# Kernel tuning notes

Hardware: AMD Instinct MI355X
Metric: run time of the kernel (lower is better)

The kernel has to match this reference:

```python
import jax, jax.numpy as jnp
import numpy as np

N_STATE = 1024
N_HEAD = 16
HEAD_DIM = N_STATE // N_HEAD
SEQLENS = [1024, 896, 768, 640, 512, 384, 896, 1024]  # sum = 6144
TOTAL = sum(SEQLENS)


def setup_inputs() -> dict:
    key = jax.random.key(0)
    ks = jax.random.split(key, 8)
    s = 0.02
    cu = jnp.asarray(np.concatenate([[0], np.cumsum(SEQLENS)]), dtype=jnp.int32)
    return {
        "x": jax.random.normal(ks[0], (TOTAL, N_STATE), jnp.float32),
        "cu_seqlens": cu,
        "Wq": jax.random.normal(ks[1], (N_STATE, N_STATE), jnp.float32) * s,
        "bq": jax.random.normal(ks[2], (N_STATE,), jnp.float32) * s,
        "Wk": jax.random.normal(ks[3], (N_STATE, N_STATE), jnp.float32) * s,
        "Wv": jax.random.normal(ks[4], (N_STATE, N_STATE), jnp.float32) * s,
        "bv": jax.random.normal(ks[5], (N_STATE,), jnp.float32) * s,
        "Wo": jax.random.normal(ks[6], (N_STATE, N_STATE), jnp.float32) * s,
        "bo": jax.random.normal(ks[7], (N_STATE,), jnp.float32) * s,
    }


def reference(x, cu_seqlens, Wq, bq, Wk, Wv, bv, Wo, bo):
    # cu_seqlens is a static (host) quantity in the original (used via .tolist())
    cu = np.asarray(jax.device_get(cu_seqlens))
    seqlens = cu[1:] - cu[:-1]
    B = len(seqlens)
    Lmax = int(seqlens.max())

    q = x @ Wq.T + bq              # [T, n_state]
    k = x @ Wk.T                   # key has no bias
    v = x @ Wv.T + bv

    # static pad/unpad index maps (honoring the ragged structure)
    ar = np.arange(Lmax)
    valid = ar[None, :] < seqlens[:, None]             # [B, Lmax]
    idx = np.where(valid, cu[:-1, None] + ar[None, :], 0)
    unpad_idx = np.nonzero(valid.reshape(-1))[0]       # flat positions of real tokens
    valid_j = jnp.asarray(valid)

    def pad(t):  # [T, n_state] -> [B, Lmax, H, D], zeros in padding
        p = jnp.where(valid_j[:, :, None], t[idx], 0.0)
        return p.reshape(B, Lmax, N_HEAD, HEAD_DIM)

    qp, kp, vp = pad(q), pad(k), pad(v)
    scale = HEAD_DIM ** -0.5
    # torch adds the bool mask (True->1.0) after masked_fill(mask==0, -max):
    # valid keys get +1.0 (softmax-invariant shift), invalid keys get -finfo.max
    big_neg = jnp.finfo(x.dtype).max
    add_mask = jnp.where(valid_j, 1.0, -big_neg)[:, None, None, :]  # [B,1,1,Lmax]

    scores = jnp.einsum("bqhd,bkhd->bhqk", qp, kp) * scale + add_mask
    weights = jax.nn.softmax(scores, axis=-1)
    ctx = jnp.einsum("bhqk,bkhd->bqhd", weights, vp)   # [B, Lmax, H, D]
    ctx_flat = ctx.reshape(B * Lmax, N_STATE)[unpad_idx]  # [T, n_state]
    return ctx_flat @ Wo.T + bo
```

## Files before the change

kernel.cpp:

```cpp
#include <hip/hip_runtime.h>

typedef unsigned short u16;
typedef unsigned int u32;
typedef __attribute__((ext_vector_type(8))) short bf16x8;
typedef __attribute__((ext_vector_type(4))) float f32x4;

#define MFMA_BF16(a, b, c) __builtin_amdgcn_mfma_f32_16x16x32_bf16((a), (b), (c), 0, 0, 0)

#define QSCALE 0.18033688011112042f

__device__ __forceinline__ u16 f2bf(float f) {
    union { float f; unsigned u; } v; v.f = f;
    return (u16)((v.u + 0x7FFFu + ((v.u >> 16) & 1u)) >> 16);
}

__device__ __forceinline__ u32 pkbf(float a, float b) {
    union { float f; unsigned u; } x, y; x.f = a; y.f = b;
    return ((x.u + 0x8000u) >> 16) | ((y.u + 0x8000u) & 0xFFFF0000u);
}

__device__ __forceinline__ void async16(const void* g, void* l) {
    __builtin_amdgcn_global_load_lds(
        (const __attribute__((address_space(1))) void*)g,
        (__attribute__((address_space(3))) void*)l, 16, 0, 0);
}

__global__ __launch_bounds__(256) void cvt_all(
    const float* __restrict__ x, const float* __restrict__ Wq, const float* __restrict__ Wk,
    const float* __restrict__ Wv, const float* __restrict__ Wo,
    u16* __restrict__ xb, u16* __restrict__ Wqb, u16* __restrict__ Wkb,
    u16* __restrict__ Wvb, u16* __restrict__ Wob) {
    int b = blockIdx.x;
    const float* src; u16* dst; int base;
    if (b < 6144)      { src = x;  dst = xb;  base = b; }
    else if (b < 7168) { src = Wq; dst = Wqb; base = b - 6144; }
    else if (b < 8192) { src = Wk; dst = Wkb; base = b - 7168; }
    else if (b < 9216) { src = Wv; dst = Wvb; base = b - 8192; }
    else               { src = Wo; dst = Wob; base = b - 9216; }
    int i = base * 256 + threadIdx.x;
    float4 v = ((const float4*)src)[i];
    unsigned long long pk = (unsigned long long)f2bf(v.x)
                          | ((unsigned long long)f2bf(v.y) << 16)
                          | ((unsigned long long)f2bf(v.z) << 32)
                          | ((unsigned long long)f2bf(v.w) << 48);
    *(unsigned long long*)(dst + (size_t)i * 4) = pk;
}

__global__ __launch_bounds__(256) void gemm_qkv(
    const u16* __restrict__ xb,
    const u16* __restrict__ Wqb, const u16* __restrict__ Wkb, const u16* __restrict__ Wvb,
    const float* __restrict__ bq, const float* __restrict__ bv,
    u16* __restrict__ qb, u16* __restrict__ kb, u16* __restrict__ vbT) {
    __shared__ __align__(16) u16 As[128 * 64];
    __shared__ __align__(16) u16 Bs[128 * 64];
    const int tid = threadIdx.x;

    const int fid = blockIdx.x;
    const int xcd = fid & 7;
    const int slot = fid >> 3;
    const int mloc = slot % 6;
    const int nidx = slot / 6;
    const int m0 = (xcd * 6 + mloc) << 7;
    const int buf = nidx >> 3;
    const int n0 = (nidx & 7) << 7;
    const u16* __restrict__ W = (buf == 0) ? Wqb : (buf == 1) ? Wkb : Wvb;

    const int rr = tid >> 3;
    const int cg = tid & 7;
    const int wv = tid >> 6, lane = tid & 63, g = lane >> 4, c = lane & 15;
    const int wm = (wv & 1) << 6, wn = (wv >> 1) << 6;

    const int sw = (cg ^ (rr & 7)) << 3;
    const u16* gA[4]; const u16* gB[4];
#pragma unroll
    for (int r = 0; r < 4; ++r) {
        gA[r] = xb + (size_t)(m0 + (r << 5) + rr) * 1024 + sw;
        gB[r] = W + (size_t)(n0 + (r << 5) + rr) * 1024 + sw;
    }

    f32x4 zero = {0.f, 0.f, 0.f, 0.f};
    f32x4 acc[4][4];
#pragma unroll
    for (int i = 0; i < 4; ++i)
#pragma unroll
        for (int j = 0; j < 4; ++j) acc[i][j] = zero;

    for (int kt = 0; kt < 16; ++kt) {
        const int k0 = kt << 6;
        __syncthreads();
#pragma unroll
        for (int r = 0; r < 4; ++r) {
            async16(gA[r] + k0, &As[(r << 11) + tid * 8]);
            async16(gB[r] + k0, &Bs[(r << 11) + tid * 8]);
        }
        __syncthreads();
#pragma unroll
        for (int ks = 0; ks < 2; ++ks) {
            bf16x8 af[4], bb[4];
#pragma unroll
            for (int i = 0; i < 4; ++i) {
                int ra = wm + (i << 4) + c;
                af[i] = *(const bf16x8*)(&As[ra * 64 + ((((ks << 2) + g) ^ (ra & 7)) << 3)]);
                int rb = wn + (i << 4) + c;
                bb[i] = *(const bf16x8*)(&Bs[rb * 64 + ((((ks << 2) + g) ^ (rb & 7)) << 3)]);
            }
#pragma unroll
            for (int i = 0; i < 4; ++i)
#pragma unroll
                for (int j = 0; j < 4; ++j) acc[i][j] = MFMA_BF16(af[i], bb[j], acc[i][j]);
        }
    }

    if (buf == 0) {
#pragma unroll
        for (int j = 0; j < 4; ++j) {
            int col = n0 + wn + (j << 4) + c;
            float bias = bq[col];
#pragma unroll
            for (int i = 0; i < 4; ++i) {
                int rowb = m0 + wm + (i << 4) + (g << 2);
#pragma unroll
                for (int r = 0; r < 4; ++r)
                    qb[(size_t)(rowb + r) * 1024 + col] = f2bf((acc[i][j][r] + bias) * QSCALE);
            }
        }
    } else if (buf == 1) {
#pragma unroll
        for (int j = 0; j < 4; ++j) {
            int col = n0 + wn + (j << 4) + c;
#pragma unroll
            for (int i = 0; i < 4; ++i) {
                int rowb = m0 + wm + (i << 4) + (g << 2);
#pragma unroll
                for (int r = 0; r < 4; ++r)
                    kb[(size_t)(rowb + r) * 1024 + col] = f2bf(acc[i][j][r]);
            }
        }
    } else {
#pragma unroll
        for (int j = 0; j < 4; ++j) {
            int col = n0 + wn + (j << 4) + c;
            float bias = bv[col];
#pragma unroll
            for (int i = 0; i < 4; ++i) {
                int trow = m0 + wm + (i << 4) + (g << 2);
                unsigned long long pk =
                      (unsigned long long)f2bf(acc[i][j][0] + bias)
                    | ((unsigned long long)f2bf(acc[i][j][1] + bias) << 16)
                    | ((unsigned long long)f2bf(acc[i][j][2] + bias) << 32)
                    | ((unsigned long long)f2bf(acc[i][j][3] + bias) << 48);
                *(unsigned long long*)(vbT + (size_t)col * 6144 + trow) = pk;
            }
        }
    }
}

__global__ __launch_bounds__(256) void gemm_out(
    const u16* __restrict__ ctxb, const u16* __restrict__ Wob,
    const float* __restrict__ bo, float* __restrict__ out) {
    __shared__ __align__(16) u16 As[64 * 64];
    __shared__ __align__(16) u16 Bs[64 * 64];
    const int tid = threadIdx.x;

    const int fid = blockIdx.x;
    const int xcd = fid & 7;
    const int slot = fid >> 3;
    const int mloc = slot % 12;
    const int nidx = slot / 12;
    const int m0 = (xcd * 12 + mloc) << 6;
    const int n0 = nidx << 6;

    const int rr = tid >> 3, cg = tid & 7;
    const int wv = tid >> 6, lane = tid & 63, g = lane >> 4, c = lane & 15;
    const int wm = (wv & 1) << 5, wn = (wv >> 1) << 5;

    const int sw = (cg ^ (rr & 7)) << 3;
    const u16* gA[2]; const u16* gB[2];
#pragma unroll
    for (int r = 0; r < 2; ++r) {
        gA[r] = ctxb + (size_t)(m0 + (r << 5) + rr) * 1024 + sw;
        gB[r] = Wob + (size_t)(n0 + (r << 5) + rr) * 1024 + sw;
    }

    f32x4 zero = {0.f, 0.f, 0.f, 0.f};
    f32x4 acc[2][2];
#pragma unroll
    for (int i = 0; i < 2; ++i)
#pragma unroll
        for (int j = 0; j < 2; ++j) acc[i][j] = zero;

    for (int kt = 0; kt < 16; ++kt) {
        const int k0 = kt << 6;
        __syncthreads();
#pragma unroll
        for (int r = 0; r < 2; ++r) {
            async16(gA[r] + k0, &As[(r << 11) + tid * 8]);
            async16(gB[r] + k0, &Bs[(r << 11) + tid * 8]);
        }
        __syncthreads();
#pragma unroll
        for (int ks = 0; ks < 2; ++ks) {
            bf16x8 af[2], bb[2];
#pragma unroll
            for (int i = 0; i < 2; ++i) {
                int ra = wm + (i << 4) + c;
                af[i] = *(const bf16x8*)(&As[ra * 64 + ((((ks << 2) + g) ^ (ra & 7)) << 3)]);
                int rb = wn + (i << 4) + c;
                bb[i] = *(const bf16x8*)(&Bs[rb * 64 + ((((ks << 2) + g) ^ (rb & 7)) << 3)]);
            }
#pragma unroll
            for (int i = 0; i < 2; ++i)
#pragma unroll
                for (int j = 0; j < 2; ++j) acc[i][j] = MFMA_BF16(af[i], bb[j], acc[i][j]);
        }
    }

#pragma unroll
    for (int j = 0; j < 2; ++j) {
        int col = n0 + wn + (j << 4) + c;
        float bias = bo[col];
#pragma unroll
        for (int i = 0; i < 2; ++i) {
            int rowb = m0 + wm + (i << 4) + (g << 2);
#pragma unroll
            for (int r = 0; r < 4; ++r)
                out[(size_t)(rowb + r) * 1024 + col] = acc[i][j][r] + bias;
        }
    }
}

__global__ __launch_bounds__(256) void attn_kernel(const u16* __restrict__ qb,
                                                   const u16* __restrict__ kb,
                                                   const u16* __restrict__ vbT,
                                                   u16* __restrict__ ctxb) {
    __shared__ __align__(16) u16 Ks[128 * 64];
    __shared__ __align__(16) u16 Vs[64 * 128];
    __shared__ __align__(16) u16 Ps[4 * 2048];

    const int tid = threadIdx.x;
    const int fid = blockIdx.x;
    const int xcd = fid & 7;
    const int slot = fid >> 3;
    const int h = (xcd << 1) + (slot >= 96 ? 1 : 0);
    const int q0 = (slot % 96) << 6;

    const int cuv[9] = {0, 1024, 1920, 2688, 3328, 3840, 4224, 5120, 6144};
    int s0 = 0, e0 = 6144;
#pragma unroll
    for (int i = 1; i < 8; ++i) {
        if (q0 >= cuv[i]) s0 = cuv[i];
        if (q0 < cuv[i] && cuv[i] < e0) e0 = cuv[i];
    }
    const int ntiles = (e0 - s0) >> 7;

    const int wv = tid >> 6, lane = tid & 63, g = lane >> 4, c = lane & 15;
    const int wrow = wv << 4;

    {
        const int rr = tid >> 3, cg = tid & 7;
#pragma unroll
        for (int r = 0; r < 2; ++r) {
            int row = (r << 5) + rr;
            async16(qb + (size_t)(q0 + row) * 1024 + (h << 6) + ((cg ^ (row & 7)) << 3),
                    Ps + (r << 11) + tid * 8);
        }
    }
    __syncthreads();

    bf16x8 qf[2];
#pragma unroll
    for (int ks = 0; ks < 2; ++ks) {
        int row = wrow + c;
        qf[ks] = *(const bf16x8*)(Ps + row * 64 + ((((ks << 2) + g) ^ (row & 7)) << 3));
    }

    float m_run = -1e30f, l_run = 0.f;
    f32x4 zero = {0.f, 0.f, 0.f, 0.f};
    f32x4 oacc[4];
#pragma unroll
    for (int nt = 0; nt < 4; ++nt) oacc[nt] = zero;

    const int pbase = (wv << 11) + c * 128;
    const int c7 = c & 7;

    for (int kt = 0; kt < ntiles; ++kt) {
        const int kv0 = s0 + (kt << 7);
        __syncthreads();
        {
            const int rr = tid >> 3, cg = tid & 7;
#pragma unroll
            for (int r = 0; r < 4; ++r) {
                int row = (r << 5) + rr;
                async16(kb + (size_t)(kv0 + row) * 1024 + (h << 6) + ((cg ^ (row & 7)) << 3),
                        Ks + (r << 11) + tid * 8);
            }
            const int rr2 = tid >> 4, cg2 = tid & 15;
#pragma unroll
            for (int r = 0; r < 4; ++r) {
                int row = (r << 4) + rr2;
                async16(vbT + (size_t)((h << 6) + row) * 6144 + kv0 + ((cg2 ^ (row & 15)) << 3),
                        Vs + (r << 11) + tid * 8);
            }
        }
        __syncthreads();

        f32x4 st[8];
#pragma unroll
        for (int mt = 0; mt < 8; ++mt) st[mt] = zero;
#pragma unroll
        for (int mt = 0; mt < 8; ++mt) {
            int row = (mt << 4) + c;
            int sw = row & 7;
#pragma unroll
            for (int ks = 0; ks < 2; ++ks) {
                bf16x8 kf = *(const bf16x8*)(&Ks[row * 64 + ((((ks << 2) + g) ^ sw) << 3)]);
                st[mt] = MFMA_BF16(kf, qf[ks], st[mt]);
            }
        }

        float mx = st[0][0];
#pragma unroll
        for (int mt = 0; mt < 8; ++mt)
#pragma unroll
            for (int r = 0; r < 4; ++r) mx = fmaxf(mx, st[mt][r]);
        mx = fmaxf(mx, __shfl_xor(mx, 16, 64));
        mx = fmaxf(mx, __shfl_xor(mx, 32, 64));
        float mnew = fmaxf(m_run, mx);
        float alpha = exp2f(m_run - mnew);
        m_run = mnew;

        float rsum = 0.f;
#pragma unroll
        for (int mt = 0; mt < 8; ++mt) {
            float p0 = exp2f(st[mt][0] - mnew);
            float p1 = exp2f(st[mt][1] - mnew);
            float p2 = exp2f(st[mt][2] - mnew);
            float p3 = exp2f(st[mt][3] - mnew);
            rsum += (p0 + p1) + (p2 + p3);
            int ph = ((mt << 2) + g) ^ (c7 << 1);
            *(uint2*)(Ps + pbase + (ph << 2)) = make_uint2(pkbf(p0, p1), pkbf(p2, p3));
        }
        rsum += __shfl_xor(rsum, 16, 64);
        rsum += __shfl_xor(rsum, 32, 64);
        l_run = l_run * alpha + rsum;

        float al[4];
#pragma unroll
        for (int r = 0; r < 4; ++r) al[r] = __shfl(alpha, (g << 2) + r, 16);
#pragma unroll
        for (int nt = 0; nt < 4; ++nt)
#pragma unroll
            for (int r = 0; r < 4; ++r) oacc[nt][r] *= al[r];

#pragma unroll
        for (int ks = 0; ks < 4; ++ks) {
            int pg = ((ks << 2) + g) ^ c7;
            bf16x8 pf = *(const bf16x8*)(Ps + pbase + (pg << 3));
#pragma unroll
            for (int nt = 0; nt < 4; ++nt) {
                int vrow = (nt << 4) + c;
                bf16x8 vf = *(const bf16x8*)(&Vs[vrow * 128 + ((((ks << 2) + g) ^ (vrow & 15)) << 3)]);
                oacc[nt] = MFMA_BF16(pf, vf, oacc[nt]);
            }
        }
    }

    float inv = 1.0f / l_run;
    float invr[4];
#pragma unroll
    for (int r = 0; r < 4; ++r) invr[r] = __shfl(inv, (g << 2) + r, 16);
#pragma unroll
    for (int r = 0; r < 4; ++r) {
        size_t rowoff = (size_t)(q0 + wrow + (g << 2) + r) * 1024 + (h << 6);
#pragma unroll
        for (int nt = 0; nt < 4; ++nt)
            ctxb[rowoff + (nt << 4) + c] = f2bf(oacc[nt][r] * invr[r]);
    }
}

extern "C" void kernel_launch(void* const* d_in, const int* in_sizes, int n_in,
                              void* d_out, int out_size, void* d_ws, size_t ws_size,
                              hipStream_t stream) {
    const float* x  = (const float*)d_in[0];
    const float* Wq = (const float*)d_in[2];
    const float* bq = (const float*)d_in[3];
    const float* Wk = (const float*)d_in[4];
    const float* Wv = (const float*)d_in[5];
    const float* bv = (const float*)d_in[6];
    const float* Wo = (const float*)d_in[7];
    const float* bo = (const float*)d_in[8];
    float* out = (float*)d_out;

    u16* ws = (u16*)d_ws;
    u16* xb   = ws;
    u16* Wqb  = xb + 6291456;
    u16* Wkb  = Wqb + 1048576;
    u16* Wvb  = Wkb + 1048576;
    u16* Wob  = Wvb + 1048576;
    u16* qb   = Wob + 1048576;
    u16* kb   = qb + 6291456;
    u16* vbT  = kb + 6291456;
    u16* ctxb = xb;

    cvt_all<<<10240, 256, 0, stream>>>(x, Wq, Wk, Wv, Wo, xb, Wqb, Wkb, Wvb, Wob);
    gemm_qkv<<<1152, 256, 0, stream>>>(xb, Wqb, Wkb, Wvb, bq, bv, qb, kb, vbT);
    attn_kernel<<<1536, 256, 0, stream>>>(qb, kb, vbT, ctxb);
    gemm_out<<<1536, 256, 0, stream>>>(ctxb, Wob, bo, out);
}
```

Measured before the change: 233.5 us.

## Double-buffer LDS tiles in QKV, output GEMM and attention kernels

Each of the three main-loop kernels now holds two LDS buffers. The loads for the next K (or KV) tile are issued before the MFMA work on the current tile, and a single barrier sits at the end of each iteration. The aim is to hide global-to-LDS load latency behind compute and to drop one barrier per iteration. In exchange, LDS use per block doubles for the staged tiles (up to about 80KB in attention), which can reduce how many blocks fit on a CU.

```diff
diff --git a/kernel.cpp b/kernel.cpp
--- a/kernel.cpp
+++ b/kernel.cpp
@@ -51,8 +51,8 @@
     const u16* __restrict__ Wqb, const u16* __restrict__ Wkb, const u16* __restrict__ Wvb,
     const float* __restrict__ bq, const float* __restrict__ bv,
     u16* __restrict__ qb, u16* __restrict__ kb, u16* __restrict__ vbT) {
-    __shared__ __align__(16) u16 As[128 * 64];
-    __shared__ __align__(16) u16 Bs[128 * 64];
+    __shared__ __align__(16) u16 As[2][128 * 64];
+    __shared__ __align__(16) u16 Bs[2][128 * 64];
     const int tid = threadIdx.x;
 
     const int fid = blockIdx.x;
@@ -85,30 +85,39 @@
 #pragma unroll
         for (int j = 0; j < 4; ++j) acc[i][j] = zero;
 
+#pragma unroll
+    for (int r = 0; r < 4; ++r) {
+        async16(gA[r], &As[0][(r << 11) + tid * 8]);
+        async16(gB[r], &Bs[0][(r << 11) + tid * 8]);
+    }
+    __syncthreads();
+
     for (int kt = 0; kt < 16; ++kt) {
-        const int k0 = kt << 6;
-        __syncthreads();
-#pragma unroll
-        for (int r = 0; r < 4; ++r) {
-            async16(gA[r] + k0, &As[(r << 11) + tid * 8]);
-            async16(gB[r] + k0, &Bs[(r << 11) + tid * 8]);
-        }
-        __syncthreads();
+        const int cur = kt & 1;
+        if (kt < 15) {
+            const int k0 = (kt + 1) << 6;
+#pragma unroll
+            for (int r = 0; r < 4; ++r) {
+                async16(gA[r] + k0, &As[cur ^ 1][(r << 11) + tid * 8]);
+                async16(gB[r] + k0, &Bs[cur ^ 1][(r << 11) + tid * 8]);
+            }
+        }
 #pragma unroll
         for (int ks = 0; ks < 2; ++ks) {
             bf16x8 af[4], bb[4];
 #pragma unroll
             for (int i = 0; i < 4; ++i) {
                 int ra = wm + (i << 4) + c;
-                af[i] = *(const bf16x8*)(&As[ra * 64 + ((((ks << 2) + g) ^ (ra & 7)) << 3)]);
+                af[i] = *(const bf16x8*)(&As[cur][ra * 64 + ((((ks << 2) + g) ^ (ra & 7)) << 3)]);
                 int rb = wn + (i << 4) + c;
-                bb[i] = *(const bf16x8*)(&Bs[rb * 64 + ((((ks << 2) + g) ^ (rb & 7)) << 3)]);
+                bb[i] = *(const bf16x8*)(&Bs[cur][rb * 64 + ((((ks << 2) + g) ^ (rb & 7)) << 3)]);
             }
 #pragma unroll
             for (int i = 0; i < 4; ++i)
 #pragma unroll
                 for (int j = 0; j < 4; ++j) acc[i][j] = MFMA_BF16(af[i], bb[j], acc[i][j]);
         }
+        __syncthreads();
     }
 
     if (buf == 0) {
@@ -158,8 +167,8 @@
 __global__ __launch_bounds__(256) void gemm_out(
     const u16* __restrict__ ctxb, const u16* __restrict__ Wob,
     const float* __restrict__ bo, float* __restrict__ out) {
-    __shared__ __align__(16) u16 As[64 * 64];
-    __shared__ __align__(16) u16 Bs[64 * 64];
+    __shared__ __align__(16) u16 As[2][64 * 64];
+    __shared__ __align__(16) u16 Bs[2][64 * 64];
     const int tid = threadIdx.x;
 
     const int fid = blockIdx.x;
@@ -189,30 +198,39 @@
 #pragma unroll
         for (int j = 0; j < 2; ++j) acc[i][j] = zero;
 
+#pragma unroll
+    for (int r = 0; r < 2; ++r) {
+        async16(gA[r], &As[0][(r << 11) + tid * 8]);
+        async16(gB[r], &Bs[0][(r << 11) + tid * 8]);
+    }
+    __syncthreads();
+
     for (int kt = 0; kt < 16; ++kt) {
-        const int k0 = kt << 6;
-        __syncthreads();
-#pragma unroll
-        for (int r = 0; r < 2; ++r) {
-            async16(gA[r] + k0, &As[(r << 11) + tid * 8]);
-            async16(gB[r] + k0, &Bs[(r << 11) + tid * 8]);
-        }
-        __syncthreads();
+        const int cur = kt & 1;
+        if (kt < 15) {
+            const int k0 = (kt + 1) << 6;
+#pragma unroll
+            for (int r = 0; r < 2; ++r) {
+                async16(gA[r] + k0, &As[cur ^ 1][(r << 11) + tid * 8]);
+                async16(gB[r] + k0, &Bs[cur ^ 1][(r << 11) + tid * 8]);
+            }
+        }
 #pragma unroll
         for (int ks = 0; ks < 2; ++ks) {
             bf16x8 af[2], bb[2];
 #pragma unroll
             for (int i = 0; i < 2; ++i) {
                 int ra = wm + (i << 4) + c;
-                af[i] = *(const bf16x8*)(&As[ra * 64 + ((((ks << 2) + g) ^ (ra & 7)) << 3)]);
+                af[i] = *(const bf16x8*)(&As[cur][ra * 64 + ((((ks << 2) + g) ^ (ra & 7)) << 3)]);
                 int rb = wn + (i << 4) + c;
-                bb[i] = *(const bf16x8*)(&Bs[rb * 64 + ((((ks << 2) + g) ^ (rb & 7)) << 3)]);
+                bb[i] = *(const bf16x8*)(&Bs[cur][rb * 64 + ((((ks << 2) + g) ^ (rb & 7)) << 3)]);
             }
 #pragma unroll
             for (int i = 0; i < 2; ++i)
 #pragma unroll
                 for (int j = 0; j < 2; ++j) acc[i][j] = MFMA_BF16(af[i], bb[j], acc[i][j]);
         }
+        __syncthreads();
     }
 
 #pragma unroll
@@ -233,8 +251,8 @@
                                                    const u16* __restrict__ kb,
                                                    const u16* __restrict__ vbT,
                                                    u16* __restrict__ ctxb) {
-    __shared__ __align__(16) u16 Ks[128 * 64];
-    __shared__ __align__(16) u16 Vs[64 * 128];
+    __shared__ __align__(16) u16 Ks[2][128 * 64];
+    __shared__ __align__(16) u16 Vs[2][64 * 128];
     __shared__ __align__(16) u16 Ps[4 * 2048];
 
     const int tid = threadIdx.x;
@@ -256,6 +274,23 @@
     const int wv = tid >> 6, lane = tid & 63, g = lane >> 4, c = lane & 15;
     const int wrow = wv << 4;
 
+    auto stageKV = [&](int kv0, int b) {
+        const int rr = tid >> 3, cg = tid & 7;
+#pragma unroll
+        for (int r = 0; r < 4; ++r) {
+            int row = (r << 5) + rr;
+            async16(kb + (size_t)(kv0 + row) * 1024 + (h << 6) + ((cg ^ (row & 7)) << 3),
+                    &Ks[b][(r << 11) + tid * 8]);
+        }
+        const int rr2 = tid >> 4, cg2 = tid & 15;
+#pragma unroll
+        for (int r = 0; r < 4; ++r) {
+            int row = (r << 4) + rr2;
+            async16(vbT + (size_t)((h << 6) + row) * 6144 + kv0 + ((cg2 ^ (row & 15)) << 3),
+                    &Vs[b][(r << 11) + tid * 8]);
+        }
+    };
+
     {
         const int rr = tid >> 3, cg = tid & 7;
 #pragma unroll
@@ -264,6 +299,7 @@
             async16(qb + (size_t)(q0 + row) * 1024 + (h << 6) + ((cg ^ (row & 7)) << 3),
                     Ps + (r << 11) + tid * 8);
         }
+        stageKV(s0, 0);
     }
     __syncthreads();
 
@@ -273,6 +309,7 @@
         int row = wrow + c;
         qf[ks] = *(const bf16x8*)(Ps + row * 64 + ((((ks << 2) + g) ^ (row & 7)) << 3));
     }
+    __syncthreads();
 
     float m_run = -1e30f, l_run = 0.f;
     f32x4 zero = {0.f, 0.f, 0.f, 0.f};
@@ -284,25 +321,8 @@
     const int c7 = c & 7;
 
     for (int kt = 0; kt < ntiles; ++kt) {
-        const int kv0 = s0 + (kt << 7);
-        __syncthreads();
-        {
-            const int rr = tid >> 3, cg = tid & 7;
-#pragma unroll
-            for (int r = 0; r < 4; ++r) {
-                int row = (r << 5) + rr;
-                async16(kb + (size_t)(kv0 + row) * 1024 + (h << 6) + ((cg ^ (row & 7)) << 3),
-                        Ks + (r << 11) + tid * 8);
-            }
-            const int rr2 = tid >> 4, cg2 = tid & 15;
-#pragma unroll
-            for (int r = 0; r < 4; ++r) {
-                int row = (r << 4) + rr2;
-                async16(vbT + (size_t)((h << 6) + row) * 6144 + kv0 + ((cg2 ^ (row & 15)) << 3),
-                        Vs + (r << 11) + tid * 8);
-            }
-        }
-        __syncthreads();
+        const int cur = kt & 1;
+        if (kt + 1 < ntiles) stageKV(s0 + ((kt + 1) << 7), cur ^ 1);
 
         f32x4 st[8];
 #pragma unroll
@@ -313,7 +333,7 @@
             int sw = row & 7;
 #pragma unroll
             for (int ks = 0; ks < 2; ++ks) {
-                bf16x8 kf = *(const bf16x8*)(&Ks[row * 64 + ((((ks << 2) + g) ^ sw) << 3)]);
+                bf16x8 kf = *(const bf16x8*)(&Ks[cur][row * 64 + ((((ks << 2) + g) ^ sw) << 3)]);
                 st[mt] = MFMA_BF16(kf, qf[ks], st[mt]);
             }
         }
@@ -359,10 +379,11 @@
 #pragma unroll
             for (int nt = 0; nt < 4; ++nt) {
                 int vrow = (nt << 4) + c;
-                bf16x8 vf = *(const bf16x8*)(&Vs[vrow * 128 + ((((ks << 2) + g) ^ (vrow & 15)) << 3)]);
+                bf16x8 vf = *(const bf16x8*)(&Vs[cur][vrow * 128 + ((((ks << 2) + g) ^ (vrow & 15)) << 3)]);
                 oacc[nt] = MFMA_BF16(pf, vf, oacc[nt]);
             }
         }
+        __syncthreads();
     }
 
     float inv = 1.0f / l_run;
```

Result: slower. 250.8 us (+7.4%).
